# Performance work log

Hardware: AMD Instinct MI355X
Metric: run time of the kernel (lower is better)

Reference implementation:

```python
import jax, jax.numpy as jnp
import numpy as np


def setup_inputs() -> dict:
    key = jax.random.key(0)
    k1, k2 = jax.random.split(key)
    Xc = jax.random.normal(k1, (16384, 3), dtype=jnp.float32)
    Xt = jax.random.normal(k2, (16384, 3), dtype=jnp.float32)
    return {"Xc": Xc, "Xt": Xt}


def _sq_dists(Xc, Xt):
    # squared Euclidean distances [N, M] via the gram trick (matches cdist(p=2)**2)
    x2 = jnp.sum(Xc * Xc, axis=-1)  # [N]
    y2 = jnp.sum(Xt * Xt, axis=-1)  # [M]
    d2 = x2[:, None] + y2[None, :] - 2.0 * (Xc @ Xt.T)
    return jnp.maximum(d2, 0.0)


def reference(Xc, Xt):
    dists = _sq_dists(Xc, Xt)              # [N, M]
    min_dist_Xc = jnp.min(dists, axis=1)   # [N]
    min_dist_Xt = jnp.min(dists, axis=0)   # [M]
    return jnp.mean(min_dist_Xc) + jnp.mean(min_dist_Xt)
```

## Files before the change

### kernel.cpp

```cpp
#include <hip/hip_runtime.h>
#include <hip/hip_bf16.h>

#define BLOCK   256
#define QPT     8
#define DCHUNKS 128
#define CHUNK   128

__global__ __launch_bounds__(BLOCK) void chamfer_prep(
    const float* __restrict__ Xc, const float* __restrict__ Xt,
    float4* __restrict__ Pc, float4* __restrict__ Pt,
    unsigned* __restrict__ minC, unsigned* __restrict__ minT,
    float* __restrict__ out, int n, int m)
{
    int i = blockIdx.x * BLOCK + threadIdx.x;
    if (i == 0) out[0] = 0.0f;
    if (i < n) {
        float x = Xc[i * 3 + 0], y = Xc[i * 3 + 1], z = Xc[i * 3 + 2];
        Pc[i] = make_float4(x, y, z, x * x + y * y + z * z);
        minC[i] = 0xFFFFFFFFu;
    }
    if (i < m) {
        float x = Xt[i * 3 + 0], y = Xt[i * 3 + 1], z = Xt[i * 3 + 2];
        Pt[i] = make_float4(x, y, z, x * x + y * y + z * z);
        minT[i] = 0xFFFFFFFFu;
    }
}

__global__ __launch_bounds__(BLOCK) void chamfer_pass(
    const float4* __restrict__ Pc, const float4* __restrict__ Pt,
    unsigned* __restrict__ minC, unsigned* __restrict__ minT)
{
    __shared__ float4 tile[CHUNK];

    const float4* q;
    const float4* db;
    unsigned* minOut;
    if (blockIdx.z == 0) { q = Pc; db = Pt; minOut = minC; }
    else                 { q = Pt; db = Pc; minOut = minT; }

    const int qbase = blockIdx.x * (BLOCK * QPT);
    const int dbase = blockIdx.y * CHUNK;

    if (threadIdx.x < CHUNK) tile[threadIdx.x] = db[dbase + threadIdx.x];

    float qx2[QPT], qy2[QPT], qz2[QPT], q2[QPT], mn[QPT];
#pragma unroll
    for (int k = 0; k < QPT; ++k) {
        float4 v = q[qbase + k * BLOCK + threadIdx.x];
        qx2[k] = -2.0f * v.x;
        qy2[k] = -2.0f * v.y;
        qz2[k] = -2.0f * v.z;
        q2[k]  = v.w;
        mn[k]  = 3.4e38f;
    }
    __syncthreads();

#pragma unroll 2
    for (int j = 0; j < CHUNK; j += 2) {
        float4 p0 = tile[j];
        float4 p1 = tile[j + 1];
#pragma unroll
        for (int k = 0; k < QPT; ++k) {
            float a0 = fmaf(qx2[k], p0.x, p0.w);
            a0 = fmaf(qy2[k], p0.y, a0);
            a0 = fmaf(qz2[k], p0.z, a0);
            float a1 = fmaf(qx2[k], p1.x, p1.w);
            a1 = fmaf(qy2[k], p1.y, a1);
            a1 = fmaf(qz2[k], p1.z, a1);
            mn[k] = fminf(mn[k], fminf(a0, a1));
        }
    }

#pragma unroll
    for (int k = 0; k < QPT; ++k) {
        float d = fmaxf(mn[k] + q2[k], 0.0f);
        atomicMin(&minOut[qbase + k * BLOCK + threadIdx.x], __float_as_uint(d));
    }
}

#define RBLOCKS 128
__global__ __launch_bounds__(BLOCK) void chamfer_reduce(
    const unsigned* __restrict__ minC, const unsigned* __restrict__ minT,
    float* __restrict__ out, int n, int m)
{
    __shared__ float red[4];
    float s = 0.0f;
    const float invn = 1.0f / (float)n, invm = 1.0f / (float)m;
    for (int i = blockIdx.x * BLOCK + threadIdx.x; i < n; i += RBLOCKS * BLOCK)
        s += __uint_as_float(minC[i]) * invn;
    for (int i = blockIdx.x * BLOCK + threadIdx.x; i < m; i += RBLOCKS * BLOCK)
        s += __uint_as_float(minT[i]) * invm;

#pragma unroll
    for (int off = 32; off > 0; off >>= 1) s += __shfl_down(s, off, 64);
    int wave = threadIdx.x >> 6;
    int lane = threadIdx.x & 63;
    if (lane == 0) red[wave] = s;
    __syncthreads();
    if (threadIdx.x == 0) {
        float t = red[0] + red[1] + red[2] + red[3];
        atomicAdd(out, t);
    }
}

extern "C" void kernel_launch(void* const* d_in, const int* in_sizes, int n_in,
                              void* d_out, int out_size, void* d_ws, size_t ws_size,
                              hipStream_t stream) {
    const float* Xc = (const float*)d_in[0];
    const float* Xt = (const float*)d_in[1];
    const int n = in_sizes[0] / 3;
    const int m = in_sizes[1] / 3;

    unsigned* minC = (unsigned*)d_ws;
    unsigned* minT = minC + n;
    float4*   Pc   = (float4*)((char*)d_ws + (size_t)(n + m) * sizeof(unsigned));
    float4*   Pt   = Pc + n;
    float*    out  = (float*)d_out;

    int prepBlocks = ((n > m ? n : m) + BLOCK - 1) / BLOCK;
    chamfer_prep<<<prepBlocks, BLOCK, 0, stream>>>(Xc, Xt, Pc, Pt, minC, minT, out, n, m);

    dim3 grid(n / (BLOCK * QPT), DCHUNKS, 2);
    chamfer_pass<<<grid, BLOCK, 0, stream>>>(Pc, Pt, minC, minT);

    chamfer_reduce<<<RBLOCKS, BLOCK, 0, stream>>>(minC, minT, out, n, m);
}
```

Before: 98.40 us.

## Use packed FP32 FMA with pair-interleaved database layout in chamfer pass

Adds a second copy of each point cloud in a pair-interleaved layout (x0,x1,y0,y1,z0,z1,w0,w1), so the inner loop can compute two database distances at once with 2-wide float vector FMA and min. The aim is for CDNA to emit packed FP32 instructions and roughly halve VALU issue slots per distance. The shared tile and chunk size double while the number of database chunks is halved, which cuts atomicMin traffic. In exchange there is extra workspace and extra prep writes, and performance depends on the compiler actually emitting v_pk_fma_f32 and a packed min.

```diff
diff --git a/kernel.cpp b/kernel.cpp
--- a/kernel.cpp
+++ b/kernel.cpp
@@ -3,12 +3,15 @@
 
 #define BLOCK   256
 #define QPT     8
-#define DCHUNKS 128
-#define CHUNK   128
+#define DCHUNKS 64
+#define CHUNK   256
+
+typedef __attribute__((ext_vector_type(2))) float f32x2;
 
 __global__ __launch_bounds__(BLOCK) void chamfer_prep(
     const float* __restrict__ Xc, const float* __restrict__ Xt,
     float4* __restrict__ Pc, float4* __restrict__ Pt,
+    float* __restrict__ Tc, float* __restrict__ Tt,
     unsigned* __restrict__ minC, unsigned* __restrict__ minT,
     float* __restrict__ out, int n, int m)
 {
@@ -16,64 +19,79 @@
     if (i == 0) out[0] = 0.0f;
     if (i < n) {
         float x = Xc[i * 3 + 0], y = Xc[i * 3 + 1], z = Xc[i * 3 + 2];
-        Pc[i] = make_float4(x, y, z, x * x + y * y + z * z);
+        float w = x * x + y * y + z * z;
+        Pc[i] = make_float4(x, y, z, w);
         minC[i] = 0xFFFFFFFFu;
+        float* T = Tc + 8 * (i >> 1);
+        int l = i & 1;
+        T[0 + l] = x; T[2 + l] = y; T[4 + l] = z; T[6 + l] = w;
     }
     if (i < m) {
         float x = Xt[i * 3 + 0], y = Xt[i * 3 + 1], z = Xt[i * 3 + 2];
-        Pt[i] = make_float4(x, y, z, x * x + y * y + z * z);
+        float w = x * x + y * y + z * z;
+        Pt[i] = make_float4(x, y, z, w);
         minT[i] = 0xFFFFFFFFu;
+        float* T = Tt + 8 * (i >> 1);
+        int l = i & 1;
+        T[0 + l] = x; T[2 + l] = y; T[4 + l] = z; T[6 + l] = w;
     }
 }
 
 __global__ __launch_bounds__(BLOCK) void chamfer_pass(
     const float4* __restrict__ Pc, const float4* __restrict__ Pt,
+    const float4* __restrict__ Tc4, const float4* __restrict__ Tt4,
     unsigned* __restrict__ minC, unsigned* __restrict__ minT)
 {
     __shared__ float4 tile[CHUNK];
 
-    const float4* q;
-    const float4* db;
-    unsigned* minOut;
-    if (blockIdx.z == 0) { q = Pc; db = Pt; minOut = minC; }
-    else                 { q = Pt; db = Pc; minOut = minT; }
+    const float4* q; const float4* dbT; unsigned* minOut;
+    if (blockIdx.z == 0) { q = Pc; dbT = Tt4; minOut = minC; }
+    else                 { q = Pt; dbT = Tc4; minOut = minT; }
 
     const int qbase = blockIdx.x * (BLOCK * QPT);
     const int dbase = blockIdx.y * CHUNK;
 
-    if (threadIdx.x < CHUNK) tile[threadIdx.x] = db[dbase + threadIdx.x];
+    tile[threadIdx.x] = dbT[dbase + threadIdx.x];
 
-    float qx2[QPT], qy2[QPT], qz2[QPT], q2[QPT], mn[QPT];
+    f32x2 qx2[QPT], qy2[QPT], qz2[QPT], mn[QPT];
+    float q2[QPT];
 #pragma unroll
     for (int k = 0; k < QPT; ++k) {
         float4 v = q[qbase + k * BLOCK + threadIdx.x];
-        qx2[k] = -2.0f * v.x;
-        qy2[k] = -2.0f * v.y;
-        qz2[k] = -2.0f * v.z;
+        float ax = -2.0f * v.x, ay = -2.0f * v.y, az = -2.0f * v.z;
+        qx2[k] = (f32x2){ax, ax};
+        qy2[k] = (f32x2){ay, ay};
+        qz2[k] = (f32x2){az, az};
         q2[k]  = v.w;
-        mn[k]  = 3.4e38f;
+        mn[k]  = (f32x2){3.4e38f, 3.4e38f};
     }
     __syncthreads();
 
-#pragma unroll 2
-    for (int j = 0; j < CHUNK; j += 2) {
-        float4 p0 = tile[j];
-        float4 p1 = tile[j + 1];
+    for (int j = 0; j < CHUNK; j += 4) {
+        float4 lo0 = tile[j + 0];
+        float4 hi0 = tile[j + 1];
+        float4 lo1 = tile[j + 2];
+        float4 hi1 = tile[j + 3];
+        f32x2 px0 = {lo0.x, lo0.y}, py0 = {lo0.z, lo0.w};
+        f32x2 pz0 = {hi0.x, hi0.y}, pw0 = {hi0.z, hi0.w};
+        f32x2 px1 = {lo1.x, lo1.y}, py1 = {lo1.z, lo1.w};
+        f32x2 pz1 = {hi1.x, hi1.y}, pw1 = {hi1.z, hi1.w};
 #pragma unroll
         for (int k = 0; k < QPT; ++k) {
-            float a0 = fmaf(qx2[k], p0.x, p0.w);
-            a0 = fmaf(qy2[k], p0.y, a0);
-            a0 = fmaf(qz2[k], p0.z, a0);
-            float a1 = fmaf(qx2[k], p1.x, p1.w);
-            a1 = fmaf(qy2[k], p1.y, a1);
-            a1 = fmaf(qz2[k], p1.z, a1);
-            mn[k] = fminf(mn[k], fminf(a0, a1));
+            f32x2 a0 = __builtin_elementwise_fma(qx2[k], px0, pw0);
+            a0 = __builtin_elementwise_fma(qy2[k], py0, a0);
+            a0 = __builtin_elementwise_fma(qz2[k], pz0, a0);
+            f32x2 a1 = __builtin_elementwise_fma(qx2[k], px1, pw1);
+            a1 = __builtin_elementwise_fma(qy2[k], py1, a1);
+            a1 = __builtin_elementwise_fma(qz2[k], pz1, a1);
+            mn[k] = __builtin_elementwise_min(
+                        __builtin_elementwise_min(a0, a1), mn[k]);
         }
     }
 
 #pragma unroll
     for (int k = 0; k < QPT; ++k) {
-        float d = fmaxf(mn[k] + q2[k], 0.0f);
+        float d = fmaxf(fminf(mn[k].x, mn[k].y) + q2[k], 0.0f);
         atomicMin(&minOut[qbase + k * BLOCK + threadIdx.x], __float_as_uint(d));
     }
 }
@@ -115,13 +133,17 @@
     unsigned* minT = minC + n;
     float4*   Pc   = (float4*)((char*)d_ws + (size_t)(n + m) * sizeof(unsigned));
     float4*   Pt   = Pc + n;
+    float*    Tc   = (float*)(Pt + m);
+    float*    Tt   = Tc + (size_t)4 * n;
     float*    out  = (float*)d_out;
 
     int prepBlocks = ((n > m ? n : m) + BLOCK - 1) / BLOCK;
-    chamfer_prep<<<prepBlocks, BLOCK, 0, stream>>>(Xc, Xt, Pc, Pt, minC, minT, out, n, m);
+    chamfer_prep<<<prepBlocks, BLOCK, 0, stream>>>(
+        Xc, Xt, Pc, Pt, Tc, Tt, minC, minT, out, n, m);
 
     dim3 grid(n / (BLOCK * QPT), DCHUNKS, 2);
-    chamfer_pass<<<grid, BLOCK, 0, stream>>>(Pc, Pt, minC, minT);
+    chamfer_pass<<<grid, BLOCK, 0, stream>>>(
+        Pc, Pt, (const float4*)Tc, (const float4*)Tt, minC, minT);
 
     chamfer_reduce<<<RBLOCKS, BLOCK, 0, stream>>>(minC, minT, out, n, m);
 }
```

New measurement: 99.22 us. About the same (+0.8%).

## Stream database points through scalar loads instead of an LDS tile

Applied to the files above, without the earlier changes.

Drops the shared-memory tile and the block barrier. Each group of four database points is now read with an inline-asm s_load_dwordx16 into scalar registers, so every lane uses SGPR operands and there are no per-lane LDS reads. The database chunk doubles to 256 with half as many chunks, which halves the atomicMin traffic. The cost is a full lgkmcnt wait after every scalar load, which stalls the loop unless enough waves are resident to hide the latency.

```diff
diff --git a/kernel.cpp b/kernel.cpp
--- a/kernel.cpp
+++ b/kernel.cpp
@@ -3,8 +3,10 @@
 
 #define BLOCK   256
 #define QPT     8
-#define DCHUNKS 128
-#define CHUNK   128
+#define DCHUNKS 64
+#define CHUNK   256
+
+typedef __attribute__((ext_vector_type(16))) float f32x16;
 
 __global__ __launch_bounds__(BLOCK) void chamfer_prep(
     const float* __restrict__ Xc, const float* __restrict__ Xt,
@@ -30,18 +32,12 @@
     const float4* __restrict__ Pc, const float4* __restrict__ Pt,
     unsigned* __restrict__ minC, unsigned* __restrict__ minT)
 {
-    __shared__ float4 tile[CHUNK];
-
-    const float4* q;
-    const float4* db;
-    unsigned* minOut;
+    const float4* q; const float4* db; unsigned* minOut;
     if (blockIdx.z == 0) { q = Pc; db = Pt; minOut = minC; }
     else                 { q = Pt; db = Pc; minOut = minT; }
 
     const int qbase = blockIdx.x * (BLOCK * QPT);
     const int dbase = blockIdx.y * CHUNK;
-
-    if (threadIdx.x < CHUNK) tile[threadIdx.x] = db[dbase + threadIdx.x];
 
     float qx2[QPT], qy2[QPT], qz2[QPT], q2[QPT], mn[QPT];
 #pragma unroll
@@ -53,21 +49,35 @@
         q2[k]  = v.w;
         mn[k]  = 3.4e38f;
     }
-    __syncthreads();
 
-#pragma unroll 2
-    for (int j = 0; j < CHUNK; j += 2) {
-        float4 p0 = tile[j];
-        float4 p1 = tile[j + 1];
+    const char* dptr = (const char*)(db + dbase);
+
+    for (int j = 0; j < CHUNK; j += 4) {
+        f32x16 c;
+        asm volatile("s_load_dwordx16 %0, %1, 0x0\n\t"
+                     "s_waitcnt lgkmcnt(0)"
+                     : "=s"(c) : "s"(dptr + (size_t)j * 16));
+
+        float p0x = c[0],  p0y = c[1],  p0z = c[2],  p0w = c[3];
+        float p1x = c[4],  p1y = c[5],  p1z = c[6],  p1w = c[7];
+        float p2x = c[8],  p2y = c[9],  p2z = c[10], p2w = c[11];
+        float p3x = c[12], p3y = c[13], p3z = c[14], p3w = c[15];
+
 #pragma unroll
         for (int k = 0; k < QPT; ++k) {
-            float a0 = fmaf(qx2[k], p0.x, p0.w);
-            a0 = fmaf(qy2[k], p0.y, a0);
-            a0 = fmaf(qz2[k], p0.z, a0);
-            float a1 = fmaf(qx2[k], p1.x, p1.w);
-            a1 = fmaf(qy2[k], p1.y, a1);
-            a1 = fmaf(qz2[k], p1.z, a1);
-            mn[k] = fminf(mn[k], fminf(a0, a1));
+            float a0 = fmaf(qx2[k], p0x, p0w);
+            a0 = fmaf(qy2[k], p0y, a0);
+            a0 = fmaf(qz2[k], p0z, a0);
+            float a1 = fmaf(qx2[k], p1x, p1w);
+            a1 = fmaf(qy2[k], p1y, a1);
+            a1 = fmaf(qz2[k], p1z, a1);
+            float a2 = fmaf(qx2[k], p2x, p2w);
+            a2 = fmaf(qy2[k], p2y, a2);
+            a2 = fmaf(qz2[k], p2z, a2);
+            float a3 = fmaf(qx2[k], p3x, p3w);
+            a3 = fmaf(qy2[k], p3y, a3);
+            a3 = fmaf(qz2[k], p3z, a3);
+            mn[k] = fminf(fminf(a0, a1), fminf(fminf(a2, a3), mn[k]));
         }
     }
 
@@ -118,7 +128,8 @@
     float*    out  = (float*)d_out;
 
     int prepBlocks = ((n > m ? n : m) + BLOCK - 1) / BLOCK;
-    chamfer_prep<<<prepBlocks, BLOCK, 0, stream>>>(Xc, Xt, Pc, Pt, minC, minT, out, n, m);
+    chamfer_prep<<<prepBlocks, BLOCK, 0, stream>>>(
+        Xc, Xt, Pc, Pt, minC, minT, out, n, m);
 
     dim3 grid(n / (BLOCK * QPT), DCHUNKS, 2);
     chamfer_pass<<<grid, BLOCK, 0, stream>>>(Pc, Pt, minC, minT);
```

Result: slower. 121.1 us (+23.1%).

## Compute distance gram on MFMA with split-bf16 operands and single fused pass

Applied to the files above, without the earlier changes.

Replaces the scalar FMA distance loop with bf16 MFMA 16x16x32 tiles. Coordinates are split into hi/lo bf16 pairs so the products approximate fp32 accuracy, and the norm term is folded in via ones/extra K slots. One pass over the full distance matrix now yields both the row minima (registers plus shuffle reduction) and the column minima (per-tile atomics), instead of two separate directional passes. The point count is hardcoded to 16384, and the bf16 split may leave residual precision error.

```diff
diff --git a/kernel.cpp b/kernel.cpp
--- a/kernel.cpp
+++ b/kernel.cpp
@@ -1,95 +1,155 @@
 #include <hip/hip_runtime.h>
 #include <hip/hip_bf16.h>
 
-#define BLOCK   256
-#define QPT     8
-#define DCHUNKS 128
-#define CHUNK   128
+#define BLOCK    256
+#define RT       4
+#define ROWS_PB  256
+#define DCH      16
+#define NPTS     16384
+
+typedef __attribute__((ext_vector_type(8)))  short s16x8;
+typedef __attribute__((ext_vector_type(4)))  float f32x4;
+
+__device__ inline unsigned short bf16_rtn(float v) {
+    __hip_bfloat16 h = __float2bfloat16(v);
+    return __builtin_bit_cast(unsigned short, h);
+}
+__device__ inline float bf16_back(unsigned short u) {
+    return __bfloat162float(__builtin_bit_cast(__hip_bfloat16, u));
+}
 
 __global__ __launch_bounds__(BLOCK) void chamfer_prep(
     const float* __restrict__ Xc, const float* __restrict__ Xt,
-    float4* __restrict__ Pc, float4* __restrict__ Pt,
-    unsigned* __restrict__ minC, unsigned* __restrict__ minT,
-    float* __restrict__ out, int n, int m)
+    s16x8* __restrict__ Astream, s16x8* __restrict__ Bstream,
+    float* __restrict__ q2c,
+    unsigned* __restrict__ minQ, unsigned* __restrict__ minDb,
+    float* __restrict__ out)
 {
-    int i = blockIdx.x * BLOCK + threadIdx.x;
-    if (i == 0) out[0] = 0.0f;
-    if (i < n) {
-        float x = Xc[i * 3 + 0], y = Xc[i * 3 + 1], z = Xc[i * 3 + 2];
-        Pc[i] = make_float4(x, y, z, x * x + y * y + z * z);
-        minC[i] = 0xFFFFFFFFu;
+    int tid  = blockIdx.x * BLOCK + threadIdx.x;
+    int lane = tid & 63;
+    int rt   = tid >> 6;
+    int quad = lane >> 4;
+    int mcol = lane & 15;
+    int i    = rt * 16 + mcol;
+
+    if (tid == 0) out[0] = 0.0f;
+    if (tid < NPTS) {
+        float x = Xc[tid * 3 + 0], y = Xc[tid * 3 + 1], z = Xc[tid * 3 + 2];
+        q2c[tid]   = x * x + y * y + z * z;
+        minQ[tid]  = 0xFFFFFFFFu;
+        minDb[tid] = 0xFFFFFFFFu;
     }
-    if (i < m) {
+
+    const unsigned short ONE = 0x3F80;
+
+    {
+        float x = -2.0f * Xc[i * 3 + 0];
+        float y = -2.0f * Xc[i * 3 + 1];
+        float z = -2.0f * Xc[i * 3 + 2];
+        unsigned short xh = bf16_rtn(x), xl = bf16_rtn(x - bf16_back(xh));
+        unsigned short yh = bf16_rtn(y), yl = bf16_rtn(y - bf16_back(yh));
+        unsigned short zh = bf16_rtn(z), zl = bf16_rtn(z - bf16_back(zh));
+        s16x8 a = (s16x8){0,0,0,0,0,0,0,0};
+        if (quad == 0) a = (s16x8){(short)xh,(short)xh,(short)xl,(short)yh,
+                                   (short)yh,(short)yl,(short)zh,(short)zh};
+        if (quad == 1) a = (s16x8){(short)zl,(short)ONE,(short)ONE,0,0,0,0,0};
+        Astream[tid] = a;
+    }
+    {
         float x = Xt[i * 3 + 0], y = Xt[i * 3 + 1], z = Xt[i * 3 + 2];
-        Pt[i] = make_float4(x, y, z, x * x + y * y + z * z);
-        minT[i] = 0xFFFFFFFFu;
+        float p2 = x * x + y * y + z * z;
+        unsigned short xh = bf16_rtn(x), xl = bf16_rtn(x - bf16_back(xh));
+        unsigned short yh = bf16_rtn(y), yl = bf16_rtn(y - bf16_back(yh));
+        unsigned short zh = bf16_rtn(z), zl = bf16_rtn(z - bf16_back(zh));
+        unsigned short ph = bf16_rtn(p2), pl = bf16_rtn(p2 - bf16_back(ph));
+        s16x8 b = (s16x8){0,0,0,0,0,0,0,0};
+        if (quad == 0) b = (s16x8){(short)xh,(short)xl,(short)xh,(short)yh,
+                                   (short)yl,(short)yh,(short)zh,(short)zl};
+        if (quad == 1) b = (s16x8){(short)zh,(short)ph,(short)pl,0,0,0,0,0};
+        Bstream[tid] = b;
     }
 }
 
-__global__ __launch_bounds__(BLOCK) void chamfer_pass(
-    const float4* __restrict__ Pc, const float4* __restrict__ Pt,
-    unsigned* __restrict__ minC, unsigned* __restrict__ minT)
+__global__ __launch_bounds__(BLOCK, 4) void chamfer_gram(
+    const s16x8* __restrict__ Astream, const s16x8* __restrict__ Bstream,
+    const float* __restrict__ q2c,
+    unsigned* __restrict__ minQ, unsigned* __restrict__ minDb)
 {
-    __shared__ float4 tile[CHUNK];
+    const int lane = threadIdx.x & 63;
+    const int wave = threadIdx.x >> 6;
+    const int quad = lane >> 4;
 
-    const float4* q;
-    const float4* db;
-    unsigned* minOut;
-    if (blockIdx.z == 0) { q = Pc; db = Pt; minOut = minC; }
-    else                 { q = Pt; db = Pc; minOut = minT; }
+    const int rowTile0 = blockIdx.x * (ROWS_PB / 16) + wave * RT;
+    const int colTile0 = blockIdx.y * (NPTS / DCH / 16);
+    const int nColT    = NPTS / DCH / 16;
 
-    const int qbase = blockIdx.x * (BLOCK * QPT);
-    const int dbase = blockIdx.y * CHUNK;
+    s16x8 afrag[RT];
+    f32x4 q2r[RT];
+    f32x4 rowmin[RT];
+#pragma unroll
+    for (int r = 0; r < RT; ++r) {
+        afrag[r]  = Astream[(rowTile0 + r) * 64 + lane];
+        q2r[r]    = *(const f32x4*)&q2c[(rowTile0 + r) * 16 + quad * 4];
+        rowmin[r] = (f32x4){3.4e38f, 3.4e38f, 3.4e38f, 3.4e38f};
+    }
 
-    if (threadIdx.x < CHUNK) tile[threadIdx.x] = db[dbase + threadIdx.x];
+    const s16x8* Bp = Bstream + (size_t)colTile0 * 64 + lane;
 
-    float qx2[QPT], qy2[QPT], qz2[QPT], q2[QPT], mn[QPT];
+    for (int t = 0; t < nColT; ++t) {
+        s16x8 b = Bp[t * 64];
+
+        f32x4 g[RT];
 #pragma unroll
-    for (int k = 0; k < QPT; ++k) {
-        float4 v = q[qbase + k * BLOCK + threadIdx.x];
-        qx2[k] = -2.0f * v.x;
-        qy2[k] = -2.0f * v.y;
-        qz2[k] = -2.0f * v.z;
-        q2[k]  = v.w;
-        mn[k]  = 3.4e38f;
-    }
-    __syncthreads();
+        for (int r = 0; r < RT; ++r)
+            g[r] = __builtin_amdgcn_mfma_f32_16x16x32_bf16(
+                       afrag[r], b, (f32x4){0.f, 0.f, 0.f, 0.f}, 0, 0, 0);
 
-#pragma unroll 2
-    for (int j = 0; j < CHUNK; j += 2) {
-        float4 p0 = tile[j];
-        float4 p1 = tile[j + 1];
+        float cmin = 3.4e38f;
 #pragma unroll
-        for (int k = 0; k < QPT; ++k) {
-            float a0 = fmaf(qx2[k], p0.x, p0.w);
-            a0 = fmaf(qy2[k], p0.y, a0);
-            a0 = fmaf(qz2[k], p0.z, a0);
-            float a1 = fmaf(qx2[k], p1.x, p1.w);
-            a1 = fmaf(qy2[k], p1.y, a1);
-            a1 = fmaf(qz2[k], p1.z, a1);
-            mn[k] = fminf(mn[k], fminf(a0, a1));
+        for (int r = 0; r < RT; ++r) {
+            rowmin[r] = __builtin_elementwise_min(rowmin[r], g[r]);
+            f32x4 tq = g[r] + q2r[r];
+            cmin = fminf(fminf(tq.x, tq.y), fminf(fminf(tq.z, tq.w), cmin));
         }
+        cmin = fminf(cmin, __shfl_xor(cmin, 16));
+        cmin = fminf(cmin, __shfl_xor(cmin, 32));
+        if (lane < 16)
+            atomicMin(&minDb[colTile0 * 16 + t * 16 + lane],
+                      __float_as_uint(fmaxf(cmin, 0.0f)));
     }
 
 #pragma unroll
-    for (int k = 0; k < QPT; ++k) {
-        float d = fmaxf(mn[k] + q2[k], 0.0f);
-        atomicMin(&minOut[qbase + k * BLOCK + threadIdx.x], __float_as_uint(d));
+    for (int r = 0; r < RT; ++r) {
+#pragma unroll
+        for (int xm = 1; xm <= 8; xm <<= 1) {
+            rowmin[r].x = fminf(rowmin[r].x, __shfl_xor(rowmin[r].x, xm));
+            rowmin[r].y = fminf(rowmin[r].y, __shfl_xor(rowmin[r].y, xm));
+            rowmin[r].z = fminf(rowmin[r].z, __shfl_xor(rowmin[r].z, xm));
+            rowmin[r].w = fminf(rowmin[r].w, __shfl_xor(rowmin[r].w, xm));
+        }
+        if ((lane & 15) == 0) {
+            f32x4 d = rowmin[r] + q2r[r];
+            int rowb = (rowTile0 + r) * 16 + quad * 4;
+            atomicMin(&minQ[rowb + 0], __float_as_uint(fmaxf(d.x, 0.0f)));
+            atomicMin(&minQ[rowb + 1], __float_as_uint(fmaxf(d.y, 0.0f)));
+            atomicMin(&minQ[rowb + 2], __float_as_uint(fmaxf(d.z, 0.0f)));
+            atomicMin(&minQ[rowb + 3], __float_as_uint(fmaxf(d.w, 0.0f)));
+        }
     }
 }
 
 #define RBLOCKS 128
 __global__ __launch_bounds__(BLOCK) void chamfer_reduce(
-    const unsigned* __restrict__ minC, const unsigned* __restrict__ minT,
+    const unsigned* __restrict__ minQ, const unsigned* __restrict__ minDb,
     float* __restrict__ out, int n, int m)
 {
     __shared__ float red[4];
     float s = 0.0f;
     const float invn = 1.0f / (float)n, invm = 1.0f / (float)m;
     for (int i = blockIdx.x * BLOCK + threadIdx.x; i < n; i += RBLOCKS * BLOCK)
-        s += __uint_as_float(minC[i]) * invn;
+        s += __uint_as_float(minQ[i]) * invn;
     for (int i = blockIdx.x * BLOCK + threadIdx.x; i < m; i += RBLOCKS * BLOCK)
-        s += __uint_as_float(minT[i]) * invm;
+        s += __uint_as_float(minDb[i]) * invm;
 
 #pragma unroll
     for (int off = 32; off > 0; off >>= 1) s += __shfl_down(s, off, 64);
@@ -111,17 +171,18 @@
     const int n = in_sizes[0] / 3;
     const int m = in_sizes[1] / 3;
 
-    unsigned* minC = (unsigned*)d_ws;
-    unsigned* minT = minC + n;
-    float4*   Pc   = (float4*)((char*)d_ws + (size_t)(n + m) * sizeof(unsigned));
-    float4*   Pt   = Pc + n;
-    float*    out  = (float*)d_out;
+    unsigned* minQ  = (unsigned*)d_ws;
+    unsigned* minDb = minQ + n;
+    float*    q2c   = (float*)(minDb + m);
+    s16x8*    As    = (s16x8*)(q2c + n);
+    s16x8*    Bs    = As + (size_t)(NPTS / 16) * 64;
+    float*    out   = (float*)d_out;
 
-    int prepBlocks = ((n > m ? n : m) + BLOCK - 1) / BLOCK;
-    chamfer_prep<<<prepBlocks, BLOCK, 0, stream>>>(Xc, Xt, Pc, Pt, minC, minT, out, n, m);
+    chamfer_prep<<<(NPTS / 16) * 64 / BLOCK, BLOCK, 0, stream>>>(
+        Xc, Xt, As, Bs, q2c, minQ, minDb, out);
 
-    dim3 grid(n / (BLOCK * QPT), DCHUNKS, 2);
-    chamfer_pass<<<grid, BLOCK, 0, stream>>>(Pc, Pt, minC, minT);
+    dim3 grid(NPTS / ROWS_PB, DCH);
+    chamfer_gram<<<grid, BLOCK, 0, stream>>>(As, Bs, q2c, minQ, minDb);
 
-    chamfer_reduce<<<RBLOCKS, BLOCK, 0, stream>>>(minC, minT, out, n, m);
+    chamfer_reduce<<<RBLOCKS, BLOCK, 0, stream>>>(minQ, minDb, out, n, m);
 }
```

New measurement: 128.7 us. 30.8% more time.
